# Kernel optimization log

Measured on AMD Instinct MI355X. Metric: run time of the kernel, lower is better.

Reference implementation:

```python
import jax, jax.numpy as jnp
import numpy as np

B, N, D, H = 4, 2048, 256, 8
DH = D // H

def setup_inputs() -> dict:
    key = jax.random.key(0)
    ks = jax.random.split(key, 7)
    s = 1.0 / np.sqrt(DH)
    return {
        "sequences": jax.random.normal(ks[0], (B, N, D), dtype=jnp.float32),
        "Wq": jax.random.uniform(ks[1], (H, DH, DH), jnp.float32, -s, s),
        "bq": jax.random.uniform(ks[2], (H, DH), jnp.float32, -s, s),
        "Wk": jax.random.uniform(ks[3], (H, DH, DH), jnp.float32, -s, s),
        "bk": jax.random.uniform(ks[4], (H, DH), jnp.float32, -s, s),
        "Wv": jax.random.uniform(ks[5], (H, DH, DH), jnp.float32, -s, s),
        "bv": jax.random.uniform(ks[6], (H, DH), jnp.float32, -s, s),
    }

def reference(sequences, Wq, bq, Wk, bk, Wv, bv):
    # sequences: [B, N, D] -> [B, N, H, DH] (head h sees columns h*DH:(h+1)*DH)
    x = sequences.reshape(B, N, H, DH)
    # per-head Linear: y = x @ W.T + b
    q = jnp.einsum("bnhd,hed->bnhe", x, Wq) + bq
    k = jnp.einsum("bnhd,hed->bnhe", x, Wk) + bk
    v = jnp.einsum("bnhd,hed->bnhe", x, Wv) + bv
    scores = jnp.einsum("bnhe,bmhe->bhnm", q, k) / jnp.sqrt(jnp.float32(DH))
    attn = jax.nn.softmax(scores, axis=-1)  # [B, H, N, N]
    out = jnp.einsum("bhnm,bmhe->bnhe", attn, v)
    # hstack of per-head results == concat over last dim == reshape
    return out.reshape(B, N, D)
```

## Files before the change

### kernel.cpp

```cpp
#include <hip/hip_runtime.h>
#include <hip/hip_bf16.h>

typedef __bf16 bf16;
typedef __bf16 bf16x8 __attribute__((ext_vector_type(8)));
typedef __bf16 bf16x4 __attribute__((ext_vector_type(4)));
typedef float  f32x4  __attribute__((ext_vector_type(4)));

#define B_  4
#define N_  2048
#define D_  256
#define H_  8
#define DH_ 32
#define QKV_ELEMS (B_*H_*N_*DH_)

#define QSC    (0.17677669529663687f * 1.4426950408889634f)
#define NBIAS  (-17.312340490667562f)

#if __has_builtin(__builtin_amdgcn_exp2f)
__device__ inline float exp2_hw(float x) { return __builtin_amdgcn_exp2f(x); }
#else
__device__ inline float exp2_hw(float x) {
    float r; asm volatile("v_exp_f32 %0, %1" : "=v"(r) : "v"(x)); return r;
}
#endif

__device__ inline void gload_lds16(const bf16* g, bf16* l) {
    __builtin_amdgcn_global_load_lds(
        (const __attribute__((address_space(1))) void*)g,
        (__attribute__((address_space(3))) void*)l, 16, 0, 0);
}

#define WAITCNT_VM8 0x0F78

__device__ inline bf16x8 ldcvt8(const float* __restrict__ p) {
    f32x4 a = *(const f32x4*)p;
    f32x4 b = *(const f32x4*)(p + 4);
    bf16x8 r;
    r[0] = (bf16)a[0]; r[1] = (bf16)a[1]; r[2] = (bf16)a[2]; r[3] = (bf16)a[3];
    r[4] = (bf16)b[0]; r[5] = (bf16)b[1]; r[6] = (bf16)b[2]; r[7] = (bf16)b[3];
    return r;
}

__global__ __launch_bounds__(256, 4) void qkv_proj_kernel(
    const float* __restrict__ x,
    const float* __restrict__ Wq, const float* __restrict__ bq,
    const float* __restrict__ Wk, const float* __restrict__ bk,
    const float* __restrict__ Wv, const float* __restrict__ bv,
    bf16* __restrict__ Qg, bf16* __restrict__ Kg, bf16* __restrict__ Vg)
{
    const int bh = blockIdx.x & 31, nt = blockIdx.x >> 5;
    const int h  = bh & (H_-1),    b  = bh >> 3;
    const int wave = threadIdx.x >> 6, lane = threadIdx.x & 63;
    const int l16 = lane & 15, q4 = lane >> 4;
    const int n0 = nt*64 + wave*16;

    bf16x8 wqf[2], wkf[2], wvf[2];
    f32x4  bq4[2], bk4[2];
    float  bvs[2];
    #pragma unroll
    for (int half = 0; half < 2; ++half) {
        wqf[half] = ldcvt8(Wq + (h*DH_ + half*16 + l16)*DH_ + q4*8);
        wkf[half] = ldcvt8(Wk + (h*DH_ + half*16 + l16)*DH_ + q4*8);
        wvf[half] = ldcvt8(Wv + (h*DH_ + half*16 + l16)*DH_ + q4*8);
        bq4[half] = *(const f32x4*)(bq + h*DH_ + half*16 + q4*4);
        bk4[half] = *(const f32x4*)(bk + h*DH_ + half*16 + q4*4);
        bvs[half] = bv[h*DH_ + half*16 + l16];
    }

    bf16x8 xf = ldcvt8(x + ((size_t)(b*N_ + n0 + l16))*D_ + h*DH_ + q4*8);
    const f32x4 z = {0.f,0.f,0.f,0.f};

    #pragma unroll
    for (int half = 0; half < 2; ++half) {
        f32x4 dq = __builtin_amdgcn_mfma_f32_16x16x32_bf16(wqf[half], xf, z, 0, 0, 0);
        f32x4 dk = __builtin_amdgcn_mfma_f32_16x16x32_bf16(wkf[half], xf, z, 0, 0, 0);
        f32x4 dv = __builtin_amdgcn_mfma_f32_16x16x32_bf16(xf, wvf[half], z, 0, 0, 0);
        bf16x4 pq, pk, pv;
        #pragma unroll
        for (int r = 0; r < 4; ++r) {
            pq[r] = (bf16)((dq[r] + bq4[half][r]) * QSC);
            pk[r] = (bf16)(dk[r] + bk4[half][r]);
            pv[r] = (bf16)(dv[r] + bvs[half]);
        }
        const size_t row = ((size_t)bh*N_ + n0 + l16)*DH_ + half*16 + q4*4;
        *(bf16x4*)(Qg + row) = pq;
        *(bf16x4*)(Kg + row) = pk;
        const int e = half*16 + l16;
        const size_t idx = ((size_t)bh << 16) + ((size_t)(n0 >> 5) << 10)
                         + (e << 5) + (q4 << 3) + (((n0 >> 4) & 1) << 2);
        *(bf16x4*)(Vg + idx) = pv;
    }
}

__global__ __launch_bounds__(256, 2) void attn_kernel(
    const bf16* __restrict__ Qg, const bf16* __restrict__ Kg,
    const bf16* __restrict__ Vg, float* __restrict__ out)
{
    const int bh = blockIdx.x & 31;
    const int qt = blockIdx.x >> 5;
    const int h  = bh & (H_-1), b = bh >> 3;
    const int lane = threadIdx.x & 63;
    const int wave = threadIdx.x >> 6;
    const int l16 = lane & 15, q4 = lane >> 4;

    __shared__ bf16 L[4][2][4096];

    const bf16* Kb = Kg + (size_t)bh*N_*DH_;
    const bf16* Vb = Vg + ((size_t)bh << 16);
    const int qrow0 = qt*128 + wave*32;

    bf16x8 qb0 = *(const bf16x8*)(Qg + ((size_t)bh*N_ + qrow0 + l16)*DH_ + q4*8);
    bf16x8 qb1 = *(const bf16x8*)(Qg + ((size_t)bh*N_ + qrow0 + 16 + l16)*DH_ + q4*8);

    bf16x8 ones;
    #pragma unroll
    for (int j = 0; j < 8; ++j) ones[j] = (bf16)1.0f;

    f32x4 ot[2][2];
    ot[0][0] = (f32x4){0,0,0,0}; ot[0][1] = (f32x4){0,0,0,0};
    ot[1][0] = (f32x4){0,0,0,0}; ot[1][1] = (f32x4){0,0,0,0};
    f32x4 osum0 = {0,0,0,0}, osum1 = {0,0,0,0};
    const f32x4 zb = {NBIAS, NBIAS, NBIAS, NBIAS};

    const int start = ((qt*5 + bh)*4 + wave) & 31;

    {
        const bf16* gk = Kb + (size_t)start*2048;
        const bf16* gv = Vb + (size_t)start*2048;
        #pragma unroll
        for (int j = 0; j < 4; ++j) {
            gload_lds16(gk + j*512 + lane*8, &L[wave][0][j*512]);
            gload_lds16(gv + j*512 + lane*8, &L[wave][0][2048 + j*512]);
        }
    }

    for (int i = 0; i < 32; ++i) {
        const int cur = i & 1, nxt = cur ^ 1;
        const int tn = (start + i + 1) & 31;

        {
            const bf16* gk = Kb + (size_t)tn*2048;
            const bf16* gv = Vb + (size_t)tn*2048;
            #pragma unroll
            for (int j = 0; j < 4; ++j) {
                gload_lds16(gk + j*512 + lane*8, &L[wave][nxt][j*512]);
                gload_lds16(gv + j*512 + lane*8, &L[wave][nxt][2048 + j*512]);
            }
        }

        __builtin_amdgcn_s_waitcnt(WAITCNT_VM8);

        const bf16* Kc = &L[wave][cur][0];
        const bf16* Vc = &L[wave][cur][2048];

        f32x4 st[4][2];
        #pragma unroll
        for (int kc = 0; kc < 4; ++kc) {
            bf16x8 kf = *(const bf16x8*)(Kc + (kc*16 + l16)*DH_ + q4*8);
            st[kc][0] = __builtin_amdgcn_mfma_f32_16x16x32_bf16(kf, qb0, zb, 0, 0, 0);
            st[kc][1] = __builtin_amdgcn_mfma_f32_16x16x32_bf16(kf, qb1, zb, 0, 0, 0);
        }

        #pragma unroll
        for (int kk = 0; kk < 2; ++kk) {
            bf16x8 pb0, pb1;
            #pragma unroll
            for (int hf = 0; hf < 2; ++hf)
                #pragma unroll
                for (int r = 0; r < 4; ++r) {
                    pb0[hf*4 + r] = (bf16)exp2_hw(st[kk*2 + hf][0][r]);
                    pb1[hf*4 + r] = (bf16)exp2_hw(st[kk*2 + hf][1][r]);
                }
            bf16x8 v0 = *(const bf16x8*)(Vc + kk*1024 + l16*DH_ + q4*8);
            bf16x8 v1 = *(const bf16x8*)(Vc + kk*1024 + (16 + l16)*DH_ + q4*8);
            ot[0][0] = __builtin_amdgcn_mfma_f32_16x16x32_bf16(v0, pb0, ot[0][0], 0, 0, 0);
            ot[1][0] = __builtin_amdgcn_mfma_f32_16x16x32_bf16(v1, pb0, ot[1][0], 0, 0, 0);
            ot[0][1] = __builtin_amdgcn_mfma_f32_16x16x32_bf16(v0, pb1, ot[0][1], 0, 0, 0);
            ot[1][1] = __builtin_amdgcn_mfma_f32_16x16x32_bf16(v1, pb1, ot[1][1], 0, 0, 0);
            osum0 = __builtin_amdgcn_mfma_f32_16x16x32_bf16(ones, pb0, osum0, 0, 0, 0);
            osum1 = __builtin_amdgcn_mfma_f32_16x16x32_bf16(ones, pb1, osum1, 0, 0, 0);
        }
    }

    const float inv0 = 1.0f / osum0[0], inv1 = 1.0f / osum1[0];

    #pragma unroll
    for (int qh = 0; qh < 2; ++qh) {
        const float inv = qh ? inv1 : inv0;
        #pragma unroll
        for (int dhh = 0; dhh < 2; ++dhh) {
            f32x4 w;
            #pragma unroll
            for (int r = 0; r < 4; ++r) w[r] = ot[dhh][qh][r] * inv;
            *(f32x4*)(out + ((size_t)b*N_ + qrow0 + qh*16 + l16)*D_
                          + h*DH_ + dhh*16 + q4*4) = w;
        }
    }
}

extern "C" void kernel_launch(void* const* d_in, const int* in_sizes, int n_in,
                              void* d_out, int out_size, void* d_ws, size_t ws_size,
                              hipStream_t stream)
{
    const float* x  = (const float*)d_in[0];
    const float* Wq = (const float*)d_in[1];
    const float* bq = (const float*)d_in[2];
    const float* Wk = (const float*)d_in[3];
    const float* bk = (const float*)d_in[4];
    const float* Wv = (const float*)d_in[5];
    const float* bv = (const float*)d_in[6];
    float* out = (float*)d_out;

    bf16* Qg = (bf16*)d_ws;
    bf16* Kg = Qg + QKV_ELEMS;
    bf16* Vg = Kg + QKV_ELEMS;

    qkv_proj_kernel<<<dim3(B_*H_*32), dim3(256), 0, stream>>>(
        x, Wq, bq, Wk, bk, Wv, bv, Qg, Kg, Vg);
    attn_kernel<<<dim3(B_*H_*(N_/128)), dim3(256), 0, stream>>>(Qg, Kg, Vg, out);
}
```

Before: 105.0 us.

## Software-pipeline QK scores one tile ahead with triple-buffered 32-key LDS tiles

The attention loop now uses 32-key tiles in a three-slot per-wave LDS ring instead of 64-key tiles double-buffered. The QK^T MFMAs for the next tile are issued before exp2 and PV on the current tile, so exp and matrix work can overlap. Loads are now issued two tiles ahead. The cost is more loop iterations and waitcnt stalls per tile, and extra registers for the carried score tiles, which could pressure occupancy.

```diff
diff --git a/kernel.cpp b/kernel.cpp
--- a/kernel.cpp
+++ b/kernel.cpp
@@ -30,7 +30,8 @@
         (__attribute__((address_space(3))) void*)l, 16, 0, 0);
 }
 
-#define WAITCNT_VM8 0x0F78
+#define WAITCNT_VM0 0x0F70
+#define WAITCNT_VM4 0x0F74
 
 __device__ inline bf16x8 ldcvt8(const float* __restrict__ p) {
     f32x4 a = *(const f32x4*)p;
@@ -103,7 +104,7 @@
     const int wave = threadIdx.x >> 6;
     const int l16 = lane & 15, q4 = lane >> 4;
 
-    __shared__ bf16 L[4][2][4096];
+    __shared__ bf16 L[4][3][2048];
 
     const bf16* Kb = Kg + (size_t)bh*N_*DH_;
     const bf16* Vb = Vg + ((size_t)bh << 16);
@@ -122,63 +123,78 @@
     f32x4 osum0 = {0,0,0,0}, osum1 = {0,0,0,0};
     const f32x4 zb = {NBIAS, NBIAS, NBIAS, NBIAS};
 
-    const int start = ((qt*5 + bh)*4 + wave) & 31;
-
-    {
-        const bf16* gk = Kb + (size_t)start*2048;
-        const bf16* gv = Vb + (size_t)start*2048;
-        #pragma unroll
-        for (int j = 0; j < 4; ++j) {
-            gload_lds16(gk + j*512 + lane*8, &L[wave][0][j*512]);
-            gload_lds16(gv + j*512 + lane*8, &L[wave][0][2048 + j*512]);
-        }
-    }
-
-    for (int i = 0; i < 32; ++i) {
-        const int cur = i & 1, nxt = cur ^ 1;
-        const int tn = (start + i + 1) & 31;
-
-        {
-            const bf16* gk = Kb + (size_t)tn*2048;
-            const bf16* gv = Vb + (size_t)tn*2048;
+    const int start = (((qt*5 + bh)*4 + wave)*9) & 63;
+    bf16* Lw = &L[wave][0][0];
+
+    #pragma unroll
+    for (int d = 0; d < 2; ++d) {
+        const int t = (start + d) & 63;
+        const bf16* gk = Kb + (size_t)t*1024;
+        const bf16* gv = Vb + (size_t)t*1024;
+        gload_lds16(gk + lane*8,       Lw + d*2048);
+        gload_lds16(gk + 512 + lane*8, Lw + d*2048 + 512);
+        gload_lds16(gv + lane*8,       Lw + d*2048 + 1024);
+        gload_lds16(gv + 512 + lane*8, Lw + d*2048 + 1536);
+    }
+
+    __builtin_amdgcn_s_waitcnt(WAITCNT_VM4);
+    f32x4 stC[2][2];
+    #pragma unroll
+    for (int kc = 0; kc < 2; ++kc) {
+        bf16x8 kf = *(const bf16x8*)(Lw + (kc*16 + l16)*DH_ + q4*8);
+        stC[kc][0] = __builtin_amdgcn_mfma_f32_16x16x32_bf16(kf, qb0, zb, 0, 0, 0);
+        stC[kc][1] = __builtin_amdgcn_mfma_f32_16x16x32_bf16(kf, qb1, zb, 0, 0, 0);
+    }
+
+    for (int i = 0; i < 64; ++i) {
+        const int bV = i % 3;
+        const int bK = (i + 1) % 3;
+        const int bD = (i + 2) % 3;
+
+        bf16x8 v0 = *(const bf16x8*)(Lw + bV*2048 + 1024 + l16*DH_ + q4*8);
+        bf16x8 v1 = *(const bf16x8*)(Lw + bV*2048 + 1024 + (16 + l16)*DH_ + q4*8);
+
+        f32x4 stN[2][2];
+        if (i < 63) {
+            __builtin_amdgcn_s_waitcnt(WAITCNT_VM0);
+            bf16x8 kfa = *(const bf16x8*)(Lw + bK*2048 + l16*DH_ + q4*8);
+            bf16x8 kfb = *(const bf16x8*)(Lw + bK*2048 + (16 + l16)*DH_ + q4*8);
+
+            if (i < 62) {
+                const int t = (start + i + 2) & 63;
+                const bf16* gk = Kb + (size_t)t*1024;
+                const bf16* gv = Vb + (size_t)t*1024;
+                gload_lds16(gk + lane*8,       Lw + bD*2048);
+                gload_lds16(gk + 512 + lane*8, Lw + bD*2048 + 512);
+                gload_lds16(gv + lane*8,       Lw + bD*2048 + 1024);
+                gload_lds16(gv + 512 + lane*8, Lw + bD*2048 + 1536);
+            }
+
+            stN[0][0] = __builtin_amdgcn_mfma_f32_16x16x32_bf16(kfa, qb0, zb, 0, 0, 0);
+            stN[0][1] = __builtin_amdgcn_mfma_f32_16x16x32_bf16(kfa, qb1, zb, 0, 0, 0);
+            stN[1][0] = __builtin_amdgcn_mfma_f32_16x16x32_bf16(kfb, qb0, zb, 0, 0, 0);
+            stN[1][1] = __builtin_amdgcn_mfma_f32_16x16x32_bf16(kfb, qb1, zb, 0, 0, 0);
+        }
+
+        bf16x8 pb0, pb1;
+        #pragma unroll
+        for (int kc = 0; kc < 2; ++kc)
             #pragma unroll
-            for (int j = 0; j < 4; ++j) {
-                gload_lds16(gk + j*512 + lane*8, &L[wave][nxt][j*512]);
-                gload_lds16(gv + j*512 + lane*8, &L[wave][nxt][2048 + j*512]);
+            for (int r = 0; r < 4; ++r) {
+                pb0[kc*4 + r] = (bf16)exp2_hw(stC[kc][0][r]);
+                pb1[kc*4 + r] = (bf16)exp2_hw(stC[kc][1][r]);
             }
-        }
-
-        __builtin_amdgcn_s_waitcnt(WAITCNT_VM8);
-
-        const bf16* Kc = &L[wave][cur][0];
-        const bf16* Vc = &L[wave][cur][2048];
-
-        f32x4 st[4][2];
-        #pragma unroll
-        for (int kc = 0; kc < 4; ++kc) {
-            bf16x8 kf = *(const bf16x8*)(Kc + (kc*16 + l16)*DH_ + q4*8);
-            st[kc][0] = __builtin_amdgcn_mfma_f32_16x16x32_bf16(kf, qb0, zb, 0, 0, 0);
-            st[kc][1] = __builtin_amdgcn_mfma_f32_16x16x32_bf16(kf, qb1, zb, 0, 0, 0);
-        }
-
-        #pragma unroll
-        for (int kk = 0; kk < 2; ++kk) {
-            bf16x8 pb0, pb1;
-            #pragma unroll
-            for (int hf = 0; hf < 2; ++hf)
-                #pragma unroll
-                for (int r = 0; r < 4; ++r) {
-                    pb0[hf*4 + r] = (bf16)exp2_hw(st[kk*2 + hf][0][r]);
-                    pb1[hf*4 + r] = (bf16)exp2_hw(st[kk*2 + hf][1][r]);
-                }
-            bf16x8 v0 = *(const bf16x8*)(Vc + kk*1024 + l16*DH_ + q4*8);
-            bf16x8 v1 = *(const bf16x8*)(Vc + kk*1024 + (16 + l16)*DH_ + q4*8);
-            ot[0][0] = __builtin_amdgcn_mfma_f32_16x16x32_bf16(v0, pb0, ot[0][0], 0, 0, 0);
-            ot[1][0] = __builtin_amdgcn_mfma_f32_16x16x32_bf16(v1, pb0, ot[1][0], 0, 0, 0);
-            ot[0][1] = __builtin_amdgcn_mfma_f32_16x16x32_bf16(v0, pb1, ot[0][1], 0, 0, 0);
-            ot[1][1] = __builtin_amdgcn_mfma_f32_16x16x32_bf16(v1, pb1, ot[1][1], 0, 0, 0);
-            osum0 = __builtin_amdgcn_mfma_f32_16x16x32_bf16(ones, pb0, osum0, 0, 0, 0);
-            osum1 = __builtin_amdgcn_mfma_f32_16x16x32_bf16(ones, pb1, osum1, 0, 0, 0);
+        ot[0][0] = __builtin_amdgcn_mfma_f32_16x16x32_bf16(v0, pb0, ot[0][0], 0, 0, 0);
+        ot[1][0] = __builtin_amdgcn_mfma_f32_16x16x32_bf16(v1, pb0, ot[1][0], 0, 0, 0);
+        ot[0][1] = __builtin_amdgcn_mfma_f32_16x16x32_bf16(v0, pb1, ot[0][1], 0, 0, 0);
+        ot[1][1] = __builtin_amdgcn_mfma_f32_16x16x32_bf16(v1, pb1, ot[1][1], 0, 0, 0);
+        osum0 = __builtin_amdgcn_mfma_f32_16x16x32_bf16(ones, pb0, osum0, 0, 0, 0);
+        osum1 = __builtin_amdgcn_mfma_f32_16x16x32_bf16(ones, pb1, osum1, 0, 0, 0);
+
+        #pragma unroll
+        for (int kc = 0; kc < 2; ++kc) {
+            stC[kc][0] = stN[kc][0];
+            stC[kc][1] = stN[kc][1];
         }
     }
 
```

New measurement: 109.8 us. 4.6% more time.
